# Kernel optimization log

Hardware: AMD Instinct MI355X
Metric: run time of the kernel (lower is better)

## Reference

```python
import jax, jax.numpy as jnp
import numpy as np

B, S, D = 2, 2048, 1024
H = 16
DK = D // H
DFF = 4096
EPS = 1e-6


def rotate_half(x):
    x1, x2 = jnp.split(x, 2, axis=-1)
    return jnp.concatenate((-x2, x1), axis=-1)


def build_rope(dim, seq_len):
    inv_freq = 1.0 / (10000.0 ** (jnp.arange(0, dim, 2, dtype=jnp.float32) / dim))
    t = jnp.arange(seq_len, dtype=jnp.float32)
    freqs = jnp.einsum('i,j->ij', t, inv_freq)
    emb = jnp.concatenate((freqs, freqs), axis=-1)
    return jnp.cos(emb)[None, None], jnp.sin(emb)[None, None]  # [1,1,S,dk]


def rmsnorm(x, g):
    rms = jnp.sqrt(jnp.mean(x * x, axis=-1, keepdims=True) + EPS)
    return x / rms * g


def setup_inputs() -> dict:
    key = jax.random.key(0)
    ks = jax.random.split(key, 10)
    sc = 0.02
    x = jax.random.normal(ks[0], (B, S, D), dtype=jnp.float32)
    mask = jnp.tril(jnp.ones((S, S), dtype=jnp.int32))[None, None]  # causal [1,1,S,S]
    wq = jax.random.normal(ks[1], (D, D), dtype=jnp.float32) * sc
    wk = jax.random.normal(ks[2], (D, D), dtype=jnp.float32) * sc
    wv = jax.random.normal(ks[3], (D, D), dtype=jnp.float32) * sc
    wo = jax.random.normal(ks[4], (D, D), dtype=jnp.float32) * sc
    w1 = jax.random.normal(ks[5], (2 * DFF, D), dtype=jnp.float32) * sc
    w2 = jax.random.normal(ks[6], (D, DFF), dtype=jnp.float32) * sc
    g1 = jnp.ones((D,), dtype=jnp.float32)
    g2 = jnp.ones((D,), dtype=jnp.float32)
    return {"x": x, "mask": mask, "wq": wq, "wk": wk, "wv": wv, "wo": wo,
            "w1": w1, "w2": w2, "g1": g1, "g2": g2}


def decoder_block(x, mask, wq, wk, wv, wo, w1, w2, g1, g2):
    b, s, d = x.shape
    # --- self-attention sublayer ---
    h = rmsnorm(x, g1)
    q = (h @ wq.T).reshape(b, s, H, DK).transpose(0, 2, 1, 3)
    k = (h @ wk.T).reshape(b, s, H, DK).transpose(0, 2, 1, 3)
    v = (h @ wv.T).reshape(b, s, H, DK).transpose(0, 2, 1, 3)
    cos, sin = build_rope(DK, s)
    q = q * cos + rotate_half(q) * sin
    k = k * cos + rotate_half(k) * sin
    scores = jnp.einsum('bhqd,bhkd->bhqk', q, k) / jnp.sqrt(jnp.float32(DK))
    scores = jnp.where(mask == 0, jnp.float32(-1e9), scores)
    p = jax.nn.softmax(scores, axis=-1)
    ctx = jnp.einsum('bhqk,bhkd->bhqd', p, v)
    ctx = ctx.transpose(0, 2, 1, 3).reshape(b, s, d)
    x = x + ctx @ wo.T
    # --- SwiGLU FFN sublayer ---
    h2 = rmsnorm(x, g2)
    u = h2 @ w1.T  # [b,s,2*DFF]
    u1, u2 = jnp.split(u, 2, axis=-1)
    ffn = (u1 * jax.nn.silu(u2)) @ w2.T
    return x + ffn


def reference(x, mask, wq, wk, wv, wo, w1, w2, g1, g2):
    return decoder_block(x, mask, wq, wk, wv, wo, w1, w2, g1, g2)
```

## Files before the change

kernel.cpp:

```cpp
#include <hip/hip_runtime.h>
#include <hip/hip_bf16.h>

#define BB 2
#define SS 2048
#define DD 1024
#define NH 16
#define DKH 64
#define DFF 4096
#define MTOK (BB*SS)

typedef __hip_bfloat16 bf16;
typedef __attribute__((ext_vector_type(8))) short s16x8;
typedef __attribute__((ext_vector_type(4))) float f32x4;

__device__ __forceinline__ float bs2f(short s) {
    unsigned int u = ((unsigned int)(unsigned short)s) << 16;
    return __uint_as_float(u);
}
__device__ __forceinline__ float b2f(bf16 v) { return __bfloat162float(v); }
__device__ __forceinline__ bf16 f2b(float v) { return __float2bfloat16(v); }
__device__ __forceinline__ short f2bs(float v) {
    bf16 b = __float2bfloat16(v);
    return *(short*)&b;
}

__device__ __forceinline__ void load16(const bf16* g, bf16* l) {
    __builtin_amdgcn_global_load_lds((const __attribute__((address_space(1))) void*)g,
                                     (__attribute__((address_space(3))) void*)l,
                                     16, 0, 0);
}


__global__ void cvt_kernel(const float* __restrict__ src, bf16* __restrict__ dst) {
    const int i = blockIdx.x * blockDim.x + threadIdx.x;
    float4 v = ((const float4*)src)[i];
    short4 o;
    o.x = f2bs(v.x); o.y = f2bs(v.y); o.z = f2bs(v.z); o.w = f2bs(v.w);
    ((short4*)dst)[i] = o;
}

__global__ void cvt4_kernel(const float* __restrict__ s0, const float* __restrict__ s1,
                            const float* __restrict__ s2, const float* __restrict__ s3,
                            bf16* __restrict__ dst) {
    const int z = blockIdx.z;
    const float* src = (z == 0) ? s0 : (z == 1) ? s1 : (z == 2) ? s2 : s3;
    const int i = blockIdx.x * blockDim.x + threadIdx.x;
    float4 v = ((const float4*)src)[i];
    short4 o;
    o.x = f2bs(v.x); o.y = f2bs(v.y); o.z = f2bs(v.z); o.w = f2bs(v.w);
    ((short4*)(dst + (size_t)z * DD * DD))[i] = o;
}

__global__ void rmsnorm_kernel(const float* __restrict__ x, const float* __restrict__ g,
                               bf16* __restrict__ out) {
    const int row = blockIdx.x;
    const int tid = threadIdx.x;
    float4 xv = ((const float4*)(x + (size_t)row * DD))[tid];
    float ss = xv.x*xv.x + xv.y*xv.y + xv.z*xv.z + xv.w*xv.w;
    #pragma unroll
    for (int off = 32; off > 0; off >>= 1) ss += __shfl_down(ss, off);
    __shared__ float red[4];
    const int wv = tid >> 6, lane = tid & 63;
    if (lane == 0) red[wv] = ss;
    __syncthreads();
    const float tot = red[0] + red[1] + red[2] + red[3];
    const float inv = rsqrtf(tot * (1.0f / DD) + 1e-6f);
    float4 gv = ((const float4*)g)[tid];
    short4 o;
    o.x = f2bs(xv.x * inv * gv.x);
    o.y = f2bs(xv.y * inv * gv.y);
    o.z = f2bs(xv.z * inv * gv.z);
    o.w = f2bs(xv.w * inv * gv.w);
    ((short4*)(out + (size_t)row * DD))[tid] = o;
}

__global__ __launch_bounds__(256) void gemm_qkv(const bf16* __restrict__ A,
                                                const bf16* __restrict__ Wbase,
                                                bf16* __restrict__ Obase) {
    __shared__ bf16 As[128 * 32];
    __shared__ bf16 Bs[128 * 32];
    const int tid = threadIdx.x, lane = tid & 63, wv = tid >> 6;
    const int col = lane & 15, quad = lane >> 4;
    const int wm = wv >> 1, wn = wv & 1;
    const int m0 = blockIdx.y * 128;
    const int n0 = blockIdx.x * 128;
    const bf16* W = Wbase + (size_t)blockIdx.z * DD * DD;
    bf16* C = Obase + (size_t)blockIdx.z * MTOK * DD;

    const int srow = tid >> 2;
    const int scol = (((tid & 3) ^ (srow & 3))) * 8;
    const bf16* Ag = A + (size_t)(m0 + srow) * DD + scol;
    const bf16* Wg = W + (size_t)(n0 + srow) * DD + scol;
    bf16* Asl = As + tid * 8;
    bf16* Bsl = Bs + tid * 8;
    const size_t half = (size_t)64 * DD;
    const int rg = (quad ^ (col & 3)) * 8;

    f32x4 acc[4][4] = {};
    for (int k0 = 0; k0 < DD; k0 += 32) {
        __syncthreads();
        load16(Ag + k0,        Asl);
        load16(Ag + half + k0, Asl + 2048);
        load16(Wg + k0,        Bsl);
        load16(Wg + half + k0, Bsl + 2048);
        __syncthreads();
        s16x8 af[4], bfr[4];
        #pragma unroll
        for (int t = 0; t < 4; t++) {
            af[t]  = *(const s16x8*)(As + (wm * 64 + t * 16 + col) * 32 + rg);
            bfr[t] = *(const s16x8*)(Bs + (wn * 64 + t * 16 + col) * 32 + rg);
        }
        #pragma unroll
        for (int tm = 0; tm < 4; tm++)
            #pragma unroll
            for (int tn = 0; tn < 4; tn++)
                acc[tm][tn] = __builtin_amdgcn_mfma_f32_16x16x32_bf16(af[tm], bfr[tn], acc[tm][tn], 0, 0, 0);
    }
    #pragma unroll
    for (int tm = 0; tm < 4; tm++)
        #pragma unroll
        for (int tn = 0; tn < 4; tn++)
            #pragma unroll
            for (int r = 0; r < 4; r++) {
                const int rr = m0 + wm * 64 + tm * 16 + quad * 4 + r;
                const int cc = n0 + wn * 64 + tn * 16 + col;
                C[(size_t)rr * DD + cc] = f2b(acc[tm][tn][r]);
            }
}

__global__ __launch_bounds__(256) void gemm128_atomic(const bf16* __restrict__ A,
                                                      const bf16* __restrict__ W,
                                                      float* C, int N, int K, int KC) {
    __shared__ bf16 As[128 * 32];
    __shared__ bf16 Bs[128 * 32];
    const int tid = threadIdx.x, lane = tid & 63, wv = tid >> 6;
    const int col = lane & 15, quad = lane >> 4;
    const int wm = wv >> 1, wn = wv & 1;
    const int m0 = blockIdx.y * 128;
    const int n0 = blockIdx.x * 128;
    const int koff = blockIdx.z * KC;

    const int srow = tid >> 2;
    const int scol = (((tid & 3) ^ (srow & 3))) * 8;
    const bf16* Ag = A + (size_t)(m0 + srow) * K + scol;
    const bf16* Wg = W + (size_t)(n0 + srow) * K + scol;
    bf16* Asl = As + tid * 8;
    bf16* Bsl = Bs + tid * 8;
    const size_t half = (size_t)64 * K;
    const int rg = (quad ^ (col & 3)) * 8;

    f32x4 acc[4][4] = {};
    for (int k0 = koff; k0 < koff + KC; k0 += 32) {
        __syncthreads();
        load16(Ag + k0,        Asl);
        load16(Ag + half + k0, Asl + 2048);
        load16(Wg + k0,        Bsl);
        load16(Wg + half + k0, Bsl + 2048);
        __syncthreads();
        s16x8 af[4], bfr[4];
        #pragma unroll
        for (int t = 0; t < 4; t++) {
            af[t]  = *(const s16x8*)(As + (wm * 64 + t * 16 + col) * 32 + rg);
            bfr[t] = *(const s16x8*)(Bs + (wn * 64 + t * 16 + col) * 32 + rg);
        }
        #pragma unroll
        for (int tm = 0; tm < 4; tm++)
            #pragma unroll
            for (int tn = 0; tn < 4; tn++)
                acc[tm][tn] = __builtin_amdgcn_mfma_f32_16x16x32_bf16(af[tm], bfr[tn], acc[tm][tn], 0, 0, 0);
    }
    #pragma unroll
    for (int tm = 0; tm < 4; tm++)
        #pragma unroll
        for (int tn = 0; tn < 4; tn++)
            #pragma unroll
            for (int r = 0; r < 4; r++) {
                const int rr = m0 + wm * 64 + tm * 16 + quad * 4 + r;
                const int cc = n0 + wn * 64 + tn * 16 + col;
                atomicAdd(&C[(size_t)rr * N + cc], acc[tm][tn][r]);
            }
}

__global__ __launch_bounds__(256) void gemm128_part(const bf16* __restrict__ A,
                                                    const bf16* __restrict__ W,
                                                    float* __restrict__ P,
                                                    int N, int K, int KC) {
    __shared__ bf16 As[2][128 * 32];
    __shared__ bf16 Bs[2][128 * 32];
    const int tid = threadIdx.x, lane = tid & 63, wv = tid >> 6;
    const int col = lane & 15, quad = lane >> 4;
    const int wm = wv >> 1, wn = wv & 1;
    const int m0 = blockIdx.y * 128;
    const int n0 = blockIdx.x * 128;
    const int koff = blockIdx.z * KC;
    float* Pz = P + (size_t)blockIdx.z * MTOK * N;

    const int srow = tid >> 2;
    const int scol = (((tid & 3) ^ (srow & 3))) * 8;
    const bf16* Ag = A + (size_t)(m0 + srow) * K + scol;
    const bf16* Wg = W + (size_t)(n0 + srow) * K + scol;
    const size_t half = (size_t)64 * K;
    const int rg = (quad ^ (col & 3)) * 8;

    f32x4 acc[4][4] = {};
    for (int k0 = koff; k0 < koff + KC; k0 += 64) {
        __syncthreads();
        load16(Ag + k0,             As[0] + tid * 8);
        load16(Ag + half + k0,      As[0] + tid * 8 + 2048);
        load16(Ag + k0 + 32,        As[1] + tid * 8);
        load16(Ag + half + k0 + 32, As[1] + tid * 8 + 2048);
        load16(Wg + k0,             Bs[0] + tid * 8);
        load16(Wg + half + k0,      Bs[0] + tid * 8 + 2048);
        load16(Wg + k0 + 32,        Bs[1] + tid * 8);
        load16(Wg + half + k0 + 32, Bs[1] + tid * 8 + 2048);
        __syncthreads();
        #pragma unroll
        for (int kk = 0; kk < 2; kk++) {
            s16x8 af[4], bfr[4];
            #pragma unroll
            for (int t = 0; t < 4; t++) {
                af[t]  = *(const s16x8*)(As[kk] + (wm * 64 + t * 16 + col) * 32 + rg);
                bfr[t] = *(const s16x8*)(Bs[kk] + (wn * 64 + t * 16 + col) * 32 + rg);
            }
            #pragma unroll
            for (int tm = 0; tm < 4; tm++)
                #pragma unroll
                for (int tn = 0; tn < 4; tn++)
                    acc[tm][tn] = __builtin_amdgcn_mfma_f32_16x16x32_bf16(af[tm], bfr[tn], acc[tm][tn], 0, 0, 0);
        }
    }
    #pragma unroll
    for (int tm = 0; tm < 4; tm++)
        #pragma unroll
        for (int tn = 0; tn < 4; tn++)
            #pragma unroll
            for (int r = 0; r < 4; r++) {
                const int rr = m0 + wm * 64 + tm * 16 + quad * 4 + r;
                const int cc = n0 + wn * 64 + tn * 16 + col;
                Pz[(size_t)rr * N + cc] = acc[tm][tn][r];
            }
}

__global__ __launch_bounds__(256) void reduce4_kernel(const float4* __restrict__ P,
                                                      float4* __restrict__ out) {
    const size_t n4 = (size_t)MTOK * DD / 4;
    for (size_t i = (size_t)blockIdx.x * blockDim.x + threadIdx.x; i < n4;
         i += (size_t)gridDim.x * blockDim.x) {
        float4 a = out[i];
        const float4 p0 = P[i];
        const float4 p1 = P[i + n4];
        const float4 p2 = P[i + 2 * n4];
        const float4 p3 = P[i + 3 * n4];
        a.x += p0.x + p1.x + p2.x + p3.x;
        a.y += p0.y + p1.y + p2.y + p3.y;
        a.z += p0.z + p1.z + p2.z + p3.z;
        a.w += p0.w + p1.w + p2.w + p3.w;
        out[i] = a;
    }
}

__global__ __launch_bounds__(256) void gemm64n_f32res(const bf16* __restrict__ A,
                                                      const bf16* __restrict__ W,
                                                      const float* res, float* C,
                                                      int M, int N, int K) {
    __shared__ bf16 As[128 * 32];
    __shared__ bf16 Bs[64 * 32];
    const int tid = threadIdx.x, lane = tid & 63, wv = tid >> 6;
    const int col = lane & 15, quad = lane >> 4;
    const int wm = wv >> 1, wn = wv & 1;
    const int m0 = blockIdx.y * 128;
    const int n0 = blockIdx.x * 64;

    const int srow = tid >> 2;
    const int scol = (((tid & 3) ^ (srow & 3))) * 8;
    const bf16* Ag = A + (size_t)(m0 + srow) * K + scol;
    const bf16* Wg = W + (size_t)(n0 + srow) * K + scol;
    bf16* Asl = As + tid * 8;
    bf16* Bsl = Bs + tid * 8;
    const size_t half = (size_t)64 * K;
    const int rg = (quad ^ (col & 3)) * 8;

    f32x4 acc[4][2] = {};
    for (int k0 = 0; k0 < K; k0 += 32) {
        __syncthreads();
        load16(Ag + k0,        Asl);
        load16(Ag + half + k0, Asl + 2048);
        load16(Wg + k0,        Bsl);
        __syncthreads();
        s16x8 af[4], bfr[2];
        #pragma unroll
        for (int t = 0; t < 4; t++)
            af[t] = *(const s16x8*)(As + (wm * 64 + t * 16 + col) * 32 + rg);
        #pragma unroll
        for (int t = 0; t < 2; t++)
            bfr[t] = *(const s16x8*)(Bs + (wn * 32 + t * 16 + col) * 32 + rg);
        #pragma unroll
        for (int tm = 0; tm < 4; tm++)
            #pragma unroll
            for (int tn = 0; tn < 2; tn++)
                acc[tm][tn] = __builtin_amdgcn_mfma_f32_16x16x32_bf16(af[tm], bfr[tn], acc[tm][tn], 0, 0, 0);
    }
    #pragma unroll
    for (int tm = 0; tm < 4; tm++)
        #pragma unroll
        for (int tn = 0; tn < 2; tn++)
            #pragma unroll
            for (int r = 0; r < 4; r++) {
                const int rr = m0 + wm * 64 + tm * 16 + quad * 4 + r;
                const int cc = n0 + wn * 32 + tn * 16 + col;
                C[(size_t)rr * N + cc] = acc[tm][tn][r] + res[(size_t)rr * N + cc];
            }
}

__device__ __forceinline__ void stage_sw(const bf16* Ag, const bf16* Wg0, const bf16* Wg1,
                                         bf16* Asl, bf16* Bsl, int k0) {
    load16(Ag + k0,                        Asl);
    load16(Ag + k0 + 32,                   Asl + 8192);
    load16(Ag + (size_t)128 * DD + k0,     Asl + 4096);
    load16(Ag + (size_t)128 * DD + k0 + 32, Asl + 8192 + 4096);
    load16(Wg0 + k0,                       Bsl);
    load16(Wg0 + k0 + 32,                  Bsl + 8192);
    load16(Wg1 + k0,                       Bsl + 4096);
    load16(Wg1 + k0 + 32,                  Bsl + 8192 + 4096);
}

__device__ __forceinline__ void compute_sw(const bf16* Ab, const bf16* Bb,
                                           f32x4 (*acc)[4],
                                           int wm, int wn, int col, int quad) {
    const int rg = (quad ^ (col & 3)) * 8;
    #pragma unroll
    for (int kk = 0; kk < 2; kk++) {
        const bf16* Ap = Ab + kk * 8192;
        const bf16* Bp = Bb + kk * 8192;
        s16x8 af[8], bfr[4];
        #pragma unroll
        for (int t = 0; t < 8; t++)
            af[t] = *(const s16x8*)(Ap + (wm * 128 + t * 16 + col) * 32 + rg);
        #pragma unroll
        for (int t = 0; t < 4; t++)
            bfr[t] = *(const s16x8*)(Bp + (wn * 64 + t * 16 + col) * 32 + rg);
        #pragma unroll
        for (int tm = 0; tm < 8; tm++)
            #pragma unroll
            for (int tn = 0; tn < 4; tn++)
                acc[tm][tn] = __builtin_amdgcn_mfma_f32_16x16x32_bf16(af[tm], bfr[tn], acc[tm][tn], 0, 0, 0);
    }
}

__global__ __launch_bounds__(512, 2) void gemm256_swiglu(const bf16* __restrict__ A,
                                                         const bf16* __restrict__ W,
                                                         bf16* __restrict__ G,
                                                         int ybase) {
    __shared__ bf16 As[2][2][256 * 32];
    __shared__ bf16 Bs[2][2][256 * 32];
    const int tid = threadIdx.x, lane = tid & 63, wv = tid >> 6;
    const int col = lane & 15, quad = lane >> 4;
    const int wm = wv >> 2, wn = wv & 3;
    const int m0 = (blockIdx.y + ybase) * 256;
    const int n0 = blockIdx.x * 128;

    const int srow = tid >> 2;
    const int scol = ((tid & 3) ^ (srow & 3)) * 8;
    const bf16* Ag = A + (size_t)(m0 + srow) * DD + scol;
    const int r0 = srow, r1 = srow + 128;
    const int wr0 = n0 + ((r0 >> 6) << 5) + (r0 & 31) + (((r0 >> 5) & 1) ? DFF : 0);
    const int wr1 = n0 + ((r1 >> 6) << 5) + (r1 & 31) + (((r1 >> 5) & 1) ? DFF : 0);
    const bf16* Wg0 = W + (size_t)wr0 * DD + scol;
    const bf16* Wg1 = W + (size_t)wr1 * DD + scol;
    bf16* Asl = &As[0][0][0] + tid * 8;
    bf16* Bsl = &Bs[0][0][0] + tid * 8;
    const int bufoff = 2 * 8192;

    f32x4 acc[8][4] = {};

    stage_sw(Ag, Wg0, Wg1, Asl, Bsl, 0);
    __syncthreads();
    int buf = 0;
    for (int t = 0; t < 15; t++) {
        stage_sw(Ag, Wg0, Wg1, Asl + (buf ^ 1) * bufoff, Bsl + (buf ^ 1) * bufoff,
                 (t + 1) * 64);
        compute_sw(&As[buf][0][0], &Bs[buf][0][0], acc, wm, wn, col, quad);
        __syncthreads();
        buf ^= 1;
    }
    compute_sw(&As[buf][0][0], &Bs[buf][0][0], acc, wm, wn, col, quad);

    #pragma unroll
    for (int tm = 0; tm < 8; tm++)
        #pragma unroll
        for (int tn = 0; tn < 2; tn++)
            #pragma unroll
            for (int r = 0; r < 4; r++) {
                const int rr = m0 + wm * 128 + tm * 16 + quad * 4 + r;
                const int cc = n0 + wn * 32 + tn * 16 + col;
                const float u1 = acc[tm][tn][r];
                const float u2 = acc[tm][tn + 2][r];
                const float sig = 1.0f / (1.0f + __expf(-u2));
                G[(size_t)rr * DFF + cc] = f2b(u1 * u2 * sig);
            }
}

__global__ void rope_table_kernel(float2* __restrict__ tbl) {
    const int i = blockIdx.x * blockDim.x + threadIdx.x;
    const int d = i & 31, s = i >> 5;
    const float invf = powf(10000.0f, -(float)d * (1.0f / 32.0f));
    float sn, cs;
    sincosf((float)s * invf, &sn, &cs);
    tbl[i] = make_float2(cs, sn);
}

__global__ __launch_bounds__(256) void rope_vec_kernel(bf16* __restrict__ q,
                                                       bf16* __restrict__ k,
                                                       const float2* __restrict__ tbl) {
    const int tid = threadIdx.x, lane = tid & 63, wv = tid >> 6;
    const int row = blockIdx.x * 4 + wv;
    const int s = row & (SS - 1);
    const int h = lane >> 2, dp = (lane & 3) * 8;
    const size_t base = (size_t)row * DD + h * DKH + dp;
    float2 cs[8];
    #pragma unroll
    for (int j = 0; j < 8; j++) cs[j] = tbl[s * 32 + dp + j];
    s16x8 qlo = *(const s16x8*)(q + base), qhi = *(const s16x8*)(q + base + 32);
    s16x8 klo = *(const s16x8*)(k + base), khi = *(const s16x8*)(k + base + 32);
    s16x8 qlo2, qhi2, klo2, khi2;
    #pragma unroll
    for (int j = 0; j < 8; j++) {
        float x1 = bs2f(qlo[j]), x2 = bs2f(qhi[j]);
        qlo2[j] = f2bs(x1 * cs[j].x - x2 * cs[j].y);
        qhi2[j] = f2bs(x2 * cs[j].x + x1 * cs[j].y);
        x1 = bs2f(klo[j]); x2 = bs2f(khi[j]);
        klo2[j] = f2bs(x1 * cs[j].x - x2 * cs[j].y);
        khi2[j] = f2bs(x2 * cs[j].x + x1 * cs[j].y);
    }
    *(s16x8*)(q + base) = qlo2;
    *(s16x8*)(q + base + 32) = qhi2;
    *(s16x8*)(k + base) = klo2;
    *(s16x8*)(k + base + 32) = khi2;
}

__global__ __launch_bounds__(256) void vt_transpose(const bf16* __restrict__ v,
                                                    bf16* __restrict__ vt) {
    __shared__ short tile[64][72];
    const int s0 = blockIdx.x * 64;
    const int bh = blockIdx.y;
    const int b = bh >> 4, h = bh & 15;
    const bf16* src = v + (size_t)b * SS * DD + h * DKH;
    #pragma unroll
    for (int it = 0; it < 2; it++) {
        const int sl = (threadIdx.x >> 3) + it * 32;
        const int dp = (threadIdx.x & 7) * 8;
        s16x8 val = *(const s16x8*)(src + (size_t)(s0 + sl) * DD + dp);
        *(s16x8*)&tile[sl][dp] = val;
    }
    __syncthreads();
    bf16* dst = vt + (size_t)bh * DKH * SS;
    #pragma unroll
    for (int it = 0; it < 2; it++) {
        const int dk = (threadIdx.x >> 3) + it * 32;
        const int sp = (threadIdx.x & 7) * 8;
        s16x8 o;
        #pragma unroll
        for (int j = 0; j < 8; j++) o[j] = tile[sp + j][dk];
        *(s16x8*)(dst + (size_t)dk * SS + s0 + sp) = o;
    }
}

__device__ __forceinline__ void stage_kv(const bf16* kbase, const bf16* vtbase,
                                         bf16* Kd, bf16* Vd, int kt0, int tid) {
    const int row0 = tid >> 3;
    const int gl = tid & 7;
    #pragma unroll
    for (int r = 0; r < 2; r++) {
        const int row = row0 + r * 32;
        const int g = (gl ^ (row & 7)) * 8;
        load16(kbase + (size_t)(kt0 + row) * DD + g, Kd + tid * 8 + r * 2048);
        load16(vtbase + (size_t)row * SS + kt0 + g,  Vd + tid * 8 + r * 2048);
    }
}

__device__ __forceinline__ void attn_step(const bf16* Ks, const bf16* Vs,
                                          short (*pl)[72],
                                          s16x8 qf0, s16x8 qf1,
                                          f32x4* cacc, float* lacc,
                                          int col, int quad, int kt0, int q0w,
                                          bool need_mask) {
    f32x4 s4[4] = {};
    #pragma unroll
    for (int t = 0; t < 4; t++) {
        const int key = 16 * t + col;
        const int g0 = (quad ^ (key & 7)) * 8;
        s16x8 b0 = *(const s16x8*)(Ks + key * 64 + g0);
        s16x8 b1 = *(const s16x8*)(Ks + key * 64 + (g0 ^ 32));
        s4[t] = __builtin_amdgcn_mfma_f32_16x16x32_bf16(qf0, b0, s4[t], 0, 0, 0);
        s4[t] = __builtin_amdgcn_mfma_f32_16x16x32_bf16(qf1, b1, s4[t], 0, 0, 0);
    }
    #pragma unroll
    for (int t = 0; t < 4; t++)
        #pragma unroll
        for (int r = 0; r < 4; r++) {
            float sv = s4[t][r] * 0.125f;
            if (need_mask) {
                const int key = kt0 + 16 * t + col;
                const int qq  = q0w + quad * 4 + r;
                if (key > qq) sv = -1.0e30f;
            }
            const float p = __expf(sv);
            s4[t][r] = p;
            lacc[r] += p;
        }
    #pragma unroll
    for (int t = 0; t < 4; t++)
        #pragma unroll
        for (int r = 0; r < 4; r++)
            pl[quad * 4 + r][col + 16 * t] = f2bs(s4[t][r]);
    s16x8 pf0 = *(const s16x8*)&pl[col][quad * 8];
    s16x8 pf1 = *(const s16x8*)&pl[col][32 + quad * 8];
    #pragma unroll
    for (int tn = 0; tn < 4; tn++) {
        const int dk = 16 * tn + col;
        const int g0 = (quad ^ (dk & 7)) * 8;
        s16x8 b0 = *(const s16x8*)(Vs + dk * 64 + g0);
        s16x8 b1 = *(const s16x8*)(Vs + dk * 64 + (g0 ^ 32));
        cacc[tn] = __builtin_amdgcn_mfma_f32_16x16x32_bf16(pf0, b0, cacc[tn], 0, 0, 0);
        cacc[tn] = __builtin_amdgcn_mfma_f32_16x16x32_bf16(pf1, b1, cacc[tn], 0, 0, 0);
    }
}

__device__ __forceinline__ void attn_step2(const bf16* Ks, const bf16* Vs,
                                           short (*pl)[72],
                                           s16x8 qA0, s16x8 qA1,
                                           s16x8 qB0, s16x8 qB1,
                                           f32x4* caccA, f32x4* caccB,
                                           float* lA, float* lB,
                                           int col, int quad, int kt0, int q0A,
                                           bool maskA) {
    f32x4 sA[4] = {}, sB[4] = {};
    #pragma unroll
    for (int t = 0; t < 4; t++) {
        const int key = 16 * t + col;
        const int g0 = (quad ^ (key & 7)) * 8;
        s16x8 b0 = *(const s16x8*)(Ks + key * 64 + g0);
        s16x8 b1 = *(const s16x8*)(Ks + key * 64 + (g0 ^ 32));
        sA[t] = __builtin_amdgcn_mfma_f32_16x16x32_bf16(qA0, b0, sA[t], 0, 0, 0);
        sA[t] = __builtin_amdgcn_mfma_f32_16x16x32_bf16(qA1, b1, sA[t], 0, 0, 0);
        sB[t] = __builtin_amdgcn_mfma_f32_16x16x32_bf16(qB0, b0, sB[t], 0, 0, 0);
        sB[t] = __builtin_amdgcn_mfma_f32_16x16x32_bf16(qB1, b1, sB[t], 0, 0, 0);
    }
    #pragma unroll
    for (int t = 0; t < 4; t++)
        #pragma unroll
        for (int r = 0; r < 4; r++) {
            float svA = sA[t][r] * 0.125f;
            if (maskA) {
                const int key = kt0 + 16 * t + col;
                const int qq  = q0A + quad * 4 + r;
                if (key > qq) svA = -1.0e30f;
            }
            const float pA = __expf(svA);
            sA[t][r] = pA;
            lA[r] += pA;
            const float pB = __expf(sB[t][r] * 0.125f);
            sB[t][r] = pB;
            lB[r] += pB;
        }
    #pragma unroll
    for (int t = 0; t < 4; t++)
        #pragma unroll
        for (int r = 0; r < 4; r++)
            pl[quad * 4 + r][col + 16 * t] = f2bs(sA[t][r]);
    s16x8 pA0 = *(const s16x8*)&pl[col][quad * 8];
    s16x8 pA1 = *(const s16x8*)&pl[col][32 + quad * 8];
    #pragma unroll
    for (int t = 0; t < 4; t++)
        #pragma unroll
        for (int r = 0; r < 4; r++)
            pl[quad * 4 + r][col + 16 * t] = f2bs(sB[t][r]);
    s16x8 pB0 = *(const s16x8*)&pl[col][quad * 8];
    s16x8 pB1 = *(const s16x8*)&pl[col][32 + quad * 8];
    #pragma unroll
    for (int tn = 0; tn < 4; tn++) {
        const int dk = 16 * tn + col;
        const int g0 = (quad ^ (dk & 7)) * 8;
        s16x8 b0 = *(const s16x8*)(Vs + dk * 64 + g0);
        s16x8 b1 = *(const s16x8*)(Vs + dk * 64 + (g0 ^ 32));
        caccA[tn] = __builtin_amdgcn_mfma_f32_16x16x32_bf16(pA0, b0, caccA[tn], 0, 0, 0);
        caccA[tn] = __builtin_amdgcn_mfma_f32_16x16x32_bf16(pA1, b1, caccA[tn], 0, 0, 0);
        caccB[tn] = __builtin_amdgcn_mfma_f32_16x16x32_bf16(pB0, b0, caccB[tn], 0, 0, 0);
        caccB[tn] = __builtin_amdgcn_mfma_f32_16x16x32_bf16(pB1, b1, caccB[tn], 0, 0, 0);
    }
}

__global__ __launch_bounds__(256) void attn_mfma2(const bf16* __restrict__ q,
                                                  const bf16* __restrict__ k,
                                                  const bf16* __restrict__ vt,
                                                  bf16* __restrict__ ctx) {
    __shared__ bf16 Ks[2][64 * 64];
    __shared__ bf16 Vs[2][64 * 64];
    __shared__ short plds[4][16][72];
    const int tid = threadIdx.x, lane = tid & 63, wv = tid >> 6;
    const int col = lane & 15, quad = lane >> 4;
    const int bh = blockIdx.y;
    const int b = bh >> 4, h = bh & 15;
    const int tA = blockIdx.x;
    const int tB = 31 - tA;
    const int q0A = tA * 64 + wv * 16;
    const int q0B = tB * 64 + wv * 16;

    const bf16* kbase  = k  + (size_t)b * SS * DD + h * DKH;
    const bf16* vtbase = vt + (size_t)bh * DKH * SS;

    const bf16* qrA = q + (size_t)(b * SS + q0A + col) * DD + h * DKH + quad * 8;
    const bf16* qrB = q + (size_t)(b * SS + q0B + col) * DD + h * DKH + quad * 8;
    s16x8 qfA0 = *(const s16x8*)(qrA);
    s16x8 qfA1 = *(const s16x8*)(qrA + 32);
    s16x8 qfB0 = *(const s16x8*)(qrB);
    s16x8 qfB1 = *(const s16x8*)(qrB + 32);

    f32x4 caccA[4] = {}, caccB[4] = {};
    float lA[4] = {}, lB[4] = {};

    const int last = tB;
    stage_kv(kbase, vtbase, Ks[0], Vs[0], 0, tid);
    int buf = 0;
    for (int kt = 0; kt <= last; kt++) {
        __syncthreads();
        if (kt < last)
            stage_kv(kbase, vtbase, Ks[buf ^ 1], Vs[buf ^ 1], (kt + 1) * 64, tid);
        const bf16* Kc = Ks[buf];
        const bf16* Vc = Vs[buf];
        if (kt <= tA)
            attn_step2(Kc, Vc, plds[wv], qfA0, qfA1, qfB0, qfB1,
                       caccA, caccB, lA, lB, col, quad, kt * 64, q0A, kt == tA);
        else
            attn_step(Kc, Vc, plds[wv], qfB0, qfB1, caccB, lB,
                      col, quad, kt * 64, q0B, kt == tB);
        buf ^= 1;
    }
    #pragma unroll
    for (int r = 0; r < 4; r++) {
        #pragma unroll
        for (int off = 1; off < 16; off <<= 1) {
            lA[r] += __shfl_xor(lA[r], off);
            lB[r] += __shfl_xor(lB[r], off);
        }
    }
    #pragma unroll
    for (int tn = 0; tn < 4; tn++)
        #pragma unroll
        for (int r = 0; r < 4; r++) {
            const size_t tokA = (size_t)(b * SS + q0A + quad * 4 + r);
            ctx[tokA * DD + h * DKH + 16 * tn + col] = f2b(caccA[tn][r] / lA[r]);
            const size_t tokB = (size_t)(b * SS + q0B + quad * 4 + r);
            ctx[tokB * DD + h * DKH + 16 * tn + col] = f2b(caccB[tn][r] / lB[r]);
        }
}

extern "C" void kernel_launch(void* const* d_in, const int* in_sizes, int n_in,
                              void* d_out, int out_size, void* d_ws, size_t ws_size,
                              hipStream_t stream) {
    const float* x  = (const float*)d_in[0];
    const float* wq = (const float*)d_in[2];
    const float* wk = (const float*)d_in[3];
    const float* wv = (const float*)d_in[4];
    const float* wo = (const float*)d_in[5];
    const float* w1 = (const float*)d_in[6];
    const float* w2 = (const float*)d_in[7];
    const float* g1 = (const float*)d_in[8];
    const float* g2 = (const float*)d_in[9];
    float* out = (float*)d_out;
    char* ws = (char*)d_ws;

    const size_t MB = 1024 * 1024;
    bf16* hb   = (bf16*)(ws + 0 * MB);
    bf16* qb   = (bf16*)(ws + 8 * MB);
    bf16* kb   = (bf16*)(ws + 16 * MB);
    bf16* vb   = (bf16*)(ws + 24 * MB);
    bf16* ctxb = hb;
    bf16* h2b  = hb;
    bf16* gb   = qb;
    bf16* wqb  = (bf16*)(ws + 32 * MB);
    bf16* wob  = wqb + (size_t)3 * DD * DD;
    bf16* vtb  = (bf16*)(ws + 40 * MB);
    float2* rtb = (float2*)(ws + 48 * MB);
    bf16* w1b  = (bf16*)(ws + 40 * MB);
    bf16* w2b  = (bf16*)(ws + 56 * MB);
    float* pb  = (float*)(ws + 64 * MB);
    const size_t ws_needed = 64 * MB + (size_t)4 * MTOK * DD * sizeof(float);

    cvt4_kernel<<<dim3((DD * DD / 4) / 256, 1, 4), 256, 0, stream>>>(
        wq, wk, wv, wo, wqb);

    rope_table_kernel<<<(SS * 32) / 256, 256, 0, stream>>>(rtb);

    rmsnorm_kernel<<<MTOK, 256, 0, stream>>>(x, g1, hb);
    gemm_qkv<<<dim3(DD / 128, MTOK / 128, 3), 256, 0, stream>>>(hb, wqb, qb);

    vt_transpose<<<dim3(SS / 64, BB * NH), 256, 0, stream>>>(vb, vtb);
    rope_vec_kernel<<<MTOK / 4, 256, 0, stream>>>(qb, kb, rtb);

    attn_mfma2<<<dim3(16, BB * NH), 256, 0, stream>>>(qb, kb, vtb, ctxb);

    gemm64n_f32res<<<dim3(DD / 64, MTOK / 128), 256, 0, stream>>>(
        ctxb, wob, x, out, MTOK, DD, DD);
    rmsnorm_kernel<<<MTOK, 256, 0, stream>>>(out, g2, h2b);

    cvt_kernel<<<(2 * DFF * DD / 4) / 256, 256, 0, stream>>>(w1, w1b);
    cvt_kernel<<<(DD * DFF / 4) / 256, 256, 0, stream>>>(w2, w2b);

    gemm256_swiglu<<<dim3(DFF / 128, 8), 512, 0, stream>>>(h2b, w1b, gb, 0);
    gemm256_swiglu<<<dim3(DFF / 128, 8), 512, 0, stream>>>(h2b, w1b, gb, 8);

    if (ws_size >= ws_needed) {
        gemm128_part<<<dim3(DD / 128, MTOK / 128, 4), 256, 0, stream>>>(
            gb, w2b, pb, DD, DFF, DFF / 4);
        reduce4_kernel<<<2048, 256, 0, stream>>>((const float4*)pb, (float4*)out);
    } else {
        gemm128_atomic<<<dim3(DD / 128, MTOK / 128, 2), 256, 0, stream>>>(
            gb, w2b, out, DD, DFF, DFF / 2);
    }
}
```

Baseline: 442.1 us.

## Split paired causal attention tiles into one query tile per block

Replaces the attention kernel that paired a short and a long causal query tile in each block (sharing K/V staging) with one block per query tile, doubling the grid to 32x32 blocks. Longest tiles are scheduled first via reversed blockIdx to help load balance. This raises parallelism and occupancy for the 256-CU device, at the cost of loading each K/V tile twice as often and losing the shared-staging reuse.

```diff
diff --git a/kernel.cpp b/kernel.cpp
--- a/kernel.cpp
+++ b/kernel.cpp
@@ -526,71 +526,7 @@
     }
 }
 
-__device__ __forceinline__ void attn_step2(const bf16* Ks, const bf16* Vs,
-                                           short (*pl)[72],
-                                           s16x8 qA0, s16x8 qA1,
-                                           s16x8 qB0, s16x8 qB1,
-                                           f32x4* caccA, f32x4* caccB,
-                                           float* lA, float* lB,
-                                           int col, int quad, int kt0, int q0A,
-                                           bool maskA) {
-    f32x4 sA[4] = {}, sB[4] = {};
-    #pragma unroll
-    for (int t = 0; t < 4; t++) {
-        const int key = 16 * t + col;
-        const int g0 = (quad ^ (key & 7)) * 8;
-        s16x8 b0 = *(const s16x8*)(Ks + key * 64 + g0);
-        s16x8 b1 = *(const s16x8*)(Ks + key * 64 + (g0 ^ 32));
-        sA[t] = __builtin_amdgcn_mfma_f32_16x16x32_bf16(qA0, b0, sA[t], 0, 0, 0);
-        sA[t] = __builtin_amdgcn_mfma_f32_16x16x32_bf16(qA1, b1, sA[t], 0, 0, 0);
-        sB[t] = __builtin_amdgcn_mfma_f32_16x16x32_bf16(qB0, b0, sB[t], 0, 0, 0);
-        sB[t] = __builtin_amdgcn_mfma_f32_16x16x32_bf16(qB1, b1, sB[t], 0, 0, 0);
-    }
-    #pragma unroll
-    for (int t = 0; t < 4; t++)
-        #pragma unroll
-        for (int r = 0; r < 4; r++) {
-            float svA = sA[t][r] * 0.125f;
-            if (maskA) {
-                const int key = kt0 + 16 * t + col;
-                const int qq  = q0A + quad * 4 + r;
-                if (key > qq) svA = -1.0e30f;
-            }
-            const float pA = __expf(svA);
-            sA[t][r] = pA;
-            lA[r] += pA;
-            const float pB = __expf(sB[t][r] * 0.125f);
-            sB[t][r] = pB;
-            lB[r] += pB;
-        }
-    #pragma unroll
-    for (int t = 0; t < 4; t++)
-        #pragma unroll
-        for (int r = 0; r < 4; r++)
-            pl[quad * 4 + r][col + 16 * t] = f2bs(sA[t][r]);
-    s16x8 pA0 = *(const s16x8*)&pl[col][quad * 8];
-    s16x8 pA1 = *(const s16x8*)&pl[col][32 + quad * 8];
-    #pragma unroll
-    for (int t = 0; t < 4; t++)
-        #pragma unroll
-        for (int r = 0; r < 4; r++)
-            pl[quad * 4 + r][col + 16 * t] = f2bs(sB[t][r]);
-    s16x8 pB0 = *(const s16x8*)&pl[col][quad * 8];
-    s16x8 pB1 = *(const s16x8*)&pl[col][32 + quad * 8];
-    #pragma unroll
-    for (int tn = 0; tn < 4; tn++) {
-        const int dk = 16 * tn + col;
-        const int g0 = (quad ^ (dk & 7)) * 8;
-        s16x8 b0 = *(const s16x8*)(Vs + dk * 64 + g0);
-        s16x8 b1 = *(const s16x8*)(Vs + dk * 64 + (g0 ^ 32));
-        caccA[tn] = __builtin_amdgcn_mfma_f32_16x16x32_bf16(pA0, b0, caccA[tn], 0, 0, 0);
-        caccA[tn] = __builtin_amdgcn_mfma_f32_16x16x32_bf16(pA1, b1, caccA[tn], 0, 0, 0);
-        caccB[tn] = __builtin_amdgcn_mfma_f32_16x16x32_bf16(pB0, b0, caccB[tn], 0, 0, 0);
-        caccB[tn] = __builtin_amdgcn_mfma_f32_16x16x32_bf16(pB1, b1, caccB[tn], 0, 0, 0);
-    }
-}
-
-__global__ __launch_bounds__(256) void attn_mfma2(const bf16* __restrict__ q,
+__global__ __launch_bounds__(256) void attn_mfma3(const bf16* __restrict__ q,
                                                   const bf16* __restrict__ k,
                                                   const bf16* __restrict__ vt,
                                                   bf16* __restrict__ ctx) {
@@ -601,57 +537,40 @@
     const int col = lane & 15, quad = lane >> 4;
     const int bh = blockIdx.y;
     const int b = bh >> 4, h = bh & 15;
-    const int tA = blockIdx.x;
-    const int tB = 31 - tA;
-    const int q0A = tA * 64 + wv * 16;
-    const int q0B = tB * 64 + wv * 16;
+    const int t = 31 - blockIdx.x;
+    const int q0 = t * 64 + wv * 16;
 
     const bf16* kbase  = k  + (size_t)b * SS * DD + h * DKH;
     const bf16* vtbase = vt + (size_t)bh * DKH * SS;
 
-    const bf16* qrA = q + (size_t)(b * SS + q0A + col) * DD + h * DKH + quad * 8;
-    const bf16* qrB = q + (size_t)(b * SS + q0B + col) * DD + h * DKH + quad * 8;
-    s16x8 qfA0 = *(const s16x8*)(qrA);
-    s16x8 qfA1 = *(const s16x8*)(qrA + 32);
-    s16x8 qfB0 = *(const s16x8*)(qrB);
-    s16x8 qfB1 = *(const s16x8*)(qrB + 32);
-
-    f32x4 caccA[4] = {}, caccB[4] = {};
-    float lA[4] = {}, lB[4] = {};
-
-    const int last = tB;
+    const bf16* qr = q + (size_t)(b * SS + q0 + col) * DD + h * DKH + quad * 8;
+    s16x8 qf0 = *(const s16x8*)(qr);
+    s16x8 qf1 = *(const s16x8*)(qr + 32);
+
+    f32x4 cacc[4] = {};
+    float l[4] = {};
+
     stage_kv(kbase, vtbase, Ks[0], Vs[0], 0, tid);
     int buf = 0;
-    for (int kt = 0; kt <= last; kt++) {
-        __syncthreads();
-        if (kt < last)
+    for (int kt = 0; kt <= t; kt++) {
+        __syncthreads();
+        if (kt < t)
             stage_kv(kbase, vtbase, Ks[buf ^ 1], Vs[buf ^ 1], (kt + 1) * 64, tid);
-        const bf16* Kc = Ks[buf];
-        const bf16* Vc = Vs[buf];
-        if (kt <= tA)
-            attn_step2(Kc, Vc, plds[wv], qfA0, qfA1, qfB0, qfB1,
-                       caccA, caccB, lA, lB, col, quad, kt * 64, q0A, kt == tA);
-        else
-            attn_step(Kc, Vc, plds[wv], qfB0, qfB1, caccB, lB,
-                      col, quad, kt * 64, q0B, kt == tB);
+        attn_step(Ks[buf], Vs[buf], plds[wv], qf0, qf1, cacc, l,
+                  col, quad, kt * 64, q0, kt == t);
         buf ^= 1;
     }
     #pragma unroll
-    for (int r = 0; r < 4; r++) {
-        #pragma unroll
-        for (int off = 1; off < 16; off <<= 1) {
-            lA[r] += __shfl_xor(lA[r], off);
-            lB[r] += __shfl_xor(lB[r], off);
-        }
-    }
+    for (int r = 0; r < 4; r++)
+        #pragma unroll
+        for (int off = 1; off < 16; off <<= 1)
+            l[r] += __shfl_xor(l[r], off);
     #pragma unroll
     for (int tn = 0; tn < 4; tn++)
         #pragma unroll
         for (int r = 0; r < 4; r++) {
-            const size_t tokA = (size_t)(b * SS + q0A + quad * 4 + r);
-            ctx[tokA * DD + h * DKH + 16 * tn + col] = f2b(caccA[tn][r] / lA[r]);
-            const size_t tokB = (size_t)(b * SS + q0B + quad * 4 + r);
-            ctx[tokB * DD + h * DKH + 16 * tn + col] = f2b(caccB[tn][r] / lB[r]);
+            const size_t tok = (size_t)(b * SS + q0 + quad * 4 + r);
+            ctx[tok * DD + h * DKH + 16 * tn + col] = f2b(cacc[tn][r] / l[r]);
         }
 }
 
@@ -698,7 +617,7 @@
     vt_transpose<<<dim3(SS / 64, BB * NH), 256, 0, stream>>>(vb, vtb);
     rope_vec_kernel<<<MTOK / 4, 256, 0, stream>>>(qb, kb, rtb);
 
-    attn_mfma2<<<dim3(16, BB * NH), 256, 0, stream>>>(qb, kb, vtb, ctxb);
+    attn_mfma3<<<dim3(32, BB * NH), 256, 0, stream>>>(qb, kb, vtb, ctxb);
 
     gemm64n_f32res<<<dim3(DD / 64, MTOK / 128), 256, 0, stream>>>(
         ctxb, wob, x, out, MTOK, DD, DD);
```

New measurement: 465.8 us. 1.05x slower.
